# Kernel tuning notes

Hardware: AMD Instinct MI355X
Metric: run time of the kernel (lower is better)

## Reference

```python
import jax, jax.numpy as jnp
import numpy as np
import math

D = 1024
H = 16

def setup_inputs() -> dict:
    key = jax.random.key(0)
    ks = jax.random.split(key, 8)
    N, X, T = 2, 1024, 4096
    s = 1.0 / math.sqrt(D)
    return {
        "previous_output": jax.random.normal(ks[0], (N, X, D), jnp.float32),
        "context": jax.random.normal(ks[1], (N, T, D), jnp.float32),
        "Wq": jax.random.normal(ks[2], (D, D), jnp.float32) * s,
        "bq": jnp.zeros((D,), jnp.float32),
        "Wk": jax.random.normal(ks[3], (D, D), jnp.float32) * s,
        "bk": jnp.zeros((D,), jnp.float32),
        "Wv": jax.random.normal(ks[4], (D, D), jnp.float32) * s,
        "bv": jnp.zeros((D,), jnp.float32),
    }

def reference(previous_output, context, Wq, bq, Wk, bk, Wv, bv):
    N, X, _ = previous_output.shape
    T = context.shape[1]
    hd = D // H
    # linear projections (torch Linear: x @ W.T + b)
    q = (previous_output @ Wq.T + bq).reshape(N, X, H, hd).transpose(0, 2, 1, 3)  # (N,H,X,hd)
    k = (context @ Wk.T + bk).reshape(N, T, H, hd).transpose(0, 2, 1, 3)          # (N,H,T,hd)
    v = (context @ Wv.T + bv).reshape(N, T, H, hd).transpose(0, 2, 1, 3)          # (N,H,T,hd)
    scores = jnp.einsum('nhxd,nhtd->nhxt', q, k) / jnp.sqrt(jnp.float32(hd))       # (N,H,X,T)
    attn = jax.nn.softmax(scores, axis=-1)
    out = jnp.einsum('nhxt,nhtd->nhxd', attn, v)                                   # (N,H,X,hd)
    return out.transpose(0, 2, 1, 3).reshape(N, X, D)
```

## Files before the change

### kernel.cpp

```cpp
#include <hip/hip_runtime.h>

typedef __bf16 bf16_t;
typedef __bf16 bf16x8 __attribute__((ext_vector_type(8)));
typedef __bf16 bf16x4 __attribute__((ext_vector_type(4)));
typedef float f32x4 __attribute__((ext_vector_type(4)));

#define D_MODEL 1024
#define NHEAD 16
#define HD 64
#define XLEN 1024
#define TLEN 4096
#define NBATCH 2
#define CEXP 0.18033688011112042f

typedef __attribute__((address_space(3))) bf16_t lds_bf16;
typedef const __attribute__((address_space(1))) bf16_t glb_bf16;

__global__ __launch_bounds__(256) void convert5(const float* __restrict__ prev, const float* __restrict__ ctx,
                                                const float* __restrict__ wq, const float* __restrict__ wk,
                                                const float* __restrict__ wv,
                                                bf16_t* __restrict__ prev_b, bf16_t* __restrict__ ctx_b,
                                                bf16_t* __restrict__ wq_b, bf16_t* __restrict__ wk_b,
                                                bf16_t* __restrict__ wv_b) {
    int b = blockIdx.x;
    const float* src; bf16_t* dst; int lb;
    if (b < 256)       { src = prev; dst = prev_b; lb = b; }
    else if (b < 1280) { src = ctx;  dst = ctx_b;  lb = b - 256; }
    else if (b < 1408) { src = wq;   dst = wq_b;   lb = b - 1280; }
    else if (b < 1536) { src = wk;   dst = wk_b;   lb = b - 1408; }
    else               { src = wv;   dst = wv_b;   lb = b - 1536; }
    const int base = lb * 8192 + threadIdx.x * 4;
#pragma unroll
    for (int i = 0; i < 8; ++i) {
        const int off = base + i * 1024;
        f32x4 f = *(const f32x4*)(src + off);
        bf16x4 h;
        h[0] = (bf16_t)f[0]; h[1] = (bf16_t)f[1]; h[2] = (bf16_t)f[2]; h[3] = (bf16_t)f[3];
        *(bf16x4*)(dst + off) = h;
    }
}

__global__ __launch_bounds__(256) void gemm_fused(const bf16_t* __restrict__ Xq, const bf16_t* __restrict__ Xc,
                                                  const bf16_t* __restrict__ wq, const bf16_t* __restrict__ wk,
                                                  const bf16_t* __restrict__ wv,
                                                  const float* __restrict__ bq, const float* __restrict__ bk,
                                                  const float* __restrict__ bv,
                                                  bf16_t* __restrict__ Qh, bf16_t* __restrict__ Kh,
                                                  bf16_t* __restrict__ Vt) {
    __shared__ bf16_t Ab[128][32];
    __shared__ bf16_t Bb[128][32];

    const int tid  = threadIdx.x;
    const int w    = tid >> 6;
    const int lane = tid & 63;
    const int q4   = lane >> 4;
    const int c    = lane & 15;

    const bf16_t* X; const bf16_t* W; const float* bias;
    int m0, n0, lshift, vmode;
    const int bid = blockIdx.x;
    if (bid < 128) {
        X = Xq; W = wq; bias = bq; lshift = 10; vmode = 0;
        m0 = (bid >> 3) * 128; n0 = (bid & 7) * 128;
    } else {
        const int b = bid - 128;
        const int xcd  = b & 7;
        const int s    = b >> 3;
        const int nb   = s >> 3;
        const int mgrp = s & 7;
        m0 = (mgrp * 8 + xcd) * 128;
        X = Xc; lshift = 12;
        if (nb < 8) { W = wk; bias = bk; vmode = 0; n0 = nb * 128; }
        else        { W = wv; bias = bv; vmode = 1; n0 = (nb - 8) * 128; }
    }
    const float osc = (bid < 128) ? CEXP : 1.0f;

    f32x4 acc[4][4];
#pragma unroll
    for (int i = 0; i < 4; ++i)
#pragma unroll
        for (int j = 0; j < 4; ++j) acc[i][j] = (f32x4){0.f, 0.f, 0.f, 0.f};

    const int mq = (w & 1) * 64;
    const int nq = (w >> 1) * 64;

    bf16_t* aBase = &Ab[0][0] + w * 512;
    bf16_t* bBase = &Bb[0][0] + w * 512;
    const bf16_t* gA = X + (size_t)(m0 + (tid >> 2)) * D_MODEL + (tid & 3) * 8;
    const bf16_t* gB = W + (size_t)(n0 + (tid >> 2)) * D_MODEL + (tid & 3) * 8;

    for (int kk = 0; kk < D_MODEL; kk += 32) {
        __syncthreads();
        __builtin_amdgcn_global_load_lds((glb_bf16*)(gA + kk), (lds_bf16*)aBase, 16, 0, 0);
        __builtin_amdgcn_global_load_lds((glb_bf16*)(gA + kk + (size_t)64 * D_MODEL), (lds_bf16*)(aBase + 2048), 16, 0, 0);
        __builtin_amdgcn_global_load_lds((glb_bf16*)(gB + kk), (lds_bf16*)bBase, 16, 0, 0);
        __builtin_amdgcn_global_load_lds((glb_bf16*)(gB + kk + (size_t)64 * D_MODEL), (lds_bf16*)(bBase + 2048), 16, 0, 0);
        __syncthreads();

        bf16x8 a[4], b[4];
#pragma unroll
        for (int i = 0; i < 4; ++i) a[i] = *(const bf16x8*)&Ab[mq + i * 16 + c][q4 * 8];
#pragma unroll
        for (int i = 0; i < 4; ++i) b[i] = *(const bf16x8*)&Bb[nq + i * 16 + c][q4 * 8];
#pragma unroll
        for (int mi = 0; mi < 4; ++mi)
#pragma unroll
            for (int ni = 0; ni < 4; ++ni)
                acc[mi][ni] = __builtin_amdgcn_mfma_f32_16x16x32_bf16(a[mi], b[ni], acc[mi][ni], 0, 0, 0);
    }

    float bv4[4];
#pragma unroll
    for (int ni = 0; ni < 4; ++ni) bv4[ni] = bias[n0 + nq + ni * 16 + c];

    const int headbase = (n0 + nq) >> 6;
    if (vmode == 0) {
        bf16_t* OutQK = (bid < 128) ? Qh : Kh;
        const int L = 1 << lshift;
#pragma unroll
        for (int mi = 0; mi < 4; ++mi) {
            const int mrow = m0 + mq + mi * 16 + q4 * 4;
            const int nb2  = mrow >> lshift;
            const int pos  = mrow & (L - 1);
            bf16_t* ob = OutQK + ((size_t)(nb2 * NHEAD + headbase) * L + pos) * HD;
#pragma unroll
            for (int ni = 0; ni < 4; ++ni) {
                const int d = ni * 16 + c;
#pragma unroll
                for (int r = 0; r < 4; ++r)
                    ob[(size_t)r * HD + d] = (bf16_t)((acc[mi][ni][r] + bv4[ni]) * osc);
            }
        }
    } else {
#pragma unroll
        for (int mi = 0; mi < 4; ++mi) {
            const int mrow = m0 + mq + mi * 16 + q4 * 4;
            const int nb2  = mrow >> 12;
            const int pos  = mrow & 4095;
            const int lin  = (pos & ~31) + ((pos >> 2) & 3) * 8 + ((pos >> 4) & 1) * 4;
#pragma unroll
            for (int ni = 0; ni < 4; ++ni) {
                const int d = ni * 16 + c;
                bf16x4 v4;
#pragma unroll
                for (int r = 0; r < 4; ++r) v4[r] = (bf16_t)(acc[mi][ni][r] + bv4[ni]);
                *(bf16x4*)(Vt + ((size_t)(nb2 * NHEAD + headbase) * HD + d) * TLEN + lin) = v4;
            }
        }
    }
}

__global__ __launch_bounds__(256, 4) void attn_kernel(const bf16_t* __restrict__ Qh,
                                                      const bf16_t* __restrict__ Kh,
                                                      const bf16_t* __restrict__ Vt,
                                                      bf16_t* __restrict__ Opart,
                                                      float* __restrict__ Lpart) {
    __shared__ __align__(16) char smem[32768];

    const int tid  = threadIdx.x;
    const int lane = tid & 63;
    const int w    = tid >> 6;
    const int q4   = lane >> 4;
    const int c    = lane & 15;

    const int bid = blockIdx.x;
    const int xcd = bid & 7;
    const int seq = bid >> 3;
    const int tq  = seq & 3;
    const int xb  = (seq >> 2) & 7;
    const int g   = seq >> 5;
    const int nh  = g * 8 + xcd;
    const int xw  = xb * 128 + w * 32;

    const bf16_t* __restrict__ Kb = Kh + (size_t)nh * TLEN * HD;
    const bf16_t* __restrict__ Vb = Vt + (size_t)nh * HD * TLEN;

    bf16x8 qa[2][2];
#pragma unroll
    for (int mi = 0; mi < 2; ++mi) {
        const bf16_t* qr = Qh + ((size_t)nh * XLEN + xw + mi * 16 + c) * HD + q4 * 8;
        qa[mi][0] = *(const bf16x8*)(qr);
        qa[mi][1] = *(const bf16x8*)(qr + 32);
    }

    const int sRow0 = tid >> 3,  sRow1 = 32 + (tid >> 3);
    const int sCh   = tid & 7;
    const int kCol0 = ((sCh ^ (sRow0 & 7)) * 8);
    const int kCol1 = ((sCh ^ (sRow1 & 7)) * 8);

    const int ofs0 = c * 128 + ((q4 ^ (c & 7)) * 16);
    const int ofs1 = c * 128 + (((4 + q4) ^ (c & 7)) * 16);

    f32x4 o[2][4];
#pragma unroll
    for (int i = 0; i < 2; ++i)
#pragma unroll
        for (int j = 0; j < 4; ++j) o[i][j] = (f32x4){0.f, 0.f, 0.f, 0.f};
    f32x4 lacc[2];
    lacc[0] = (f32x4){0.f, 0.f, 0.f, 0.f};
    lacc[1] = (f32x4){0.f, 0.f, 0.f, 0.f};

    bf16x8 ones8;
#pragma unroll
    for (int j = 0; j < 8; ++j) ones8[j] = (bf16_t)1.0f;

    const int t0base = tq * (TLEN / 4);

    {
        bf16_t* base = (bf16_t*)smem;
        __builtin_amdgcn_global_load_lds((glb_bf16*)(Kb + (size_t)(t0base + sRow0) * HD + kCol0), (lds_bf16*)(base + w * 512), 16, 0, 0);
        __builtin_amdgcn_global_load_lds((glb_bf16*)(Kb + (size_t)(t0base + sRow1) * HD + kCol1), (lds_bf16*)(base + 2048 + w * 512), 16, 0, 0);
        __builtin_amdgcn_global_load_lds((glb_bf16*)(Vb + (size_t)sRow0 * TLEN + t0base + kCol0), (lds_bf16*)(base + 4096 + w * 512), 16, 0, 0);
        __builtin_amdgcn_global_load_lds((glb_bf16*)(Vb + (size_t)sRow1 * TLEN + t0base + kCol1), (lds_bf16*)(base + 6144 + w * 512), 16, 0, 0);
    }

    for (int s = 0; s < 16; ++s) {
        __syncthreads();
        if (s < 15) {
            const int t1 = t0base + (s + 1) * 64;
            bf16_t* base = (bf16_t*)smem + ((s + 1) & 1) * 8192;
            __builtin_amdgcn_global_load_lds((glb_bf16*)(Kb + (size_t)(t1 + sRow0) * HD + kCol0), (lds_bf16*)(base + w * 512), 16, 0, 0);
            __builtin_amdgcn_global_load_lds((glb_bf16*)(Kb + (size_t)(t1 + sRow1) * HD + kCol1), (lds_bf16*)(base + 2048 + w * 512), 16, 0, 0);
            __builtin_amdgcn_global_load_lds((glb_bf16*)(Vb + (size_t)sRow0 * TLEN + t1 + kCol0), (lds_bf16*)(base + 4096 + w * 512), 16, 0, 0);
            __builtin_amdgcn_global_load_lds((glb_bf16*)(Vb + (size_t)sRow1 * TLEN + t1 + kCol1), (lds_bf16*)(base + 6144 + w * 512), 16, 0, 0);
        }

        const char* KtB = smem + (s & 1) * 16384;
        const char* VsB = KtB + 8192;
#pragma unroll
        for (int g32 = 0; g32 < 2; ++g32) {
            bf16x8 p8[2];
#pragma unroll
            for (int tt = 0; tt < 2; ++tt) {
                const int rofs = g32 * 4096 + tt * 2048;
                bf16x8 kb0 = *(const bf16x8*)(KtB + rofs + ofs0);
                bf16x8 kb1 = *(const bf16x8*)(KtB + rofs + ofs1);
#pragma unroll
                for (int mi = 0; mi < 2; ++mi) {
                    f32x4 sv = (f32x4){0.f, 0.f, 0.f, 0.f};
                    sv = __builtin_amdgcn_mfma_f32_16x16x32_bf16(kb0, qa[mi][0], sv, 0, 0, 0);
                    sv = __builtin_amdgcn_mfma_f32_16x16x32_bf16(kb1, qa[mi][1], sv, 0, 0, 0);
#pragma unroll
                    for (int r = 0; r < 4; ++r)
                        p8[mi][tt * 4 + r] = (bf16_t)__builtin_exp2f(sv[r]);
                }
            }
            const int vsel = g32 ? ofs1 : ofs0;
            bf16x8 va[4];
#pragma unroll
            for (int dt = 0; dt < 4; ++dt)
                va[dt] = *(const bf16x8*)(VsB + vsel + dt * 2048);
#pragma unroll
            for (int mi = 0; mi < 2; ++mi) {
#pragma unroll
                for (int dt = 0; dt < 4; ++dt)
                    o[mi][dt] = __builtin_amdgcn_mfma_f32_16x16x32_bf16(va[dt], p8[mi], o[mi][dt], 0, 0, 0);
                lacc[mi] = __builtin_amdgcn_mfma_f32_16x16x32_bf16(ones8, p8[mi], lacc[mi], 0, 0, 0);
            }
        }
    }

    __syncthreads();
    bf16_t* Ob = (bf16_t*)smem;
    float*  Lb = (float*)(smem + 16896);
#pragma unroll
    for (int mi = 0; mi < 2; ++mi) {
        if (q4 == 0) Lb[w * 32 + mi * 16 + c] = lacc[mi][0];
#pragma unroll
        for (int dt = 0; dt < 4; ++dt)
#pragma unroll
            for (int r = 0; r < 4; ++r)
                Ob[w * 2112 + (dt * 16 + q4 * 4 + r) * 33 + mi * 16 + c] = (bf16_t)o[mi][dt][r];
    }
    {
        const int lr = lane >> 1;
        const int dh = lane & 1;
        bf16x8 out4[4];
#pragma unroll
        for (int j2 = 0; j2 < 4; ++j2)
#pragma unroll
            for (int e = 0; e < 8; ++e)
                out4[j2][e] = Ob[w * 2112 + (dh * 32 + j2 * 8 + e) * 33 + lr];
        const size_t pair = (size_t)nh * XLEN + xw + lr;
        bf16_t* op = Opart + (pair * 4 + tq) * HD + dh * 32;
#pragma unroll
        for (int j2 = 0; j2 < 4; ++j2)
            *(bf16x8*)(op + j2 * 8) = out4[j2];
        if (dh == 0) Lpart[pair * 4 + tq] = Lb[w * 32 + lr];
    }
}

__global__ __launch_bounds__(256) void attn_merge(const bf16_t* __restrict__ Opart,
                                                  const float* __restrict__ Lpart,
                                                  float* __restrict__ Out) {
    const int u    = blockIdx.x * 256 + threadIdx.x;
    const int pair = u >> 3;
    const int d0   = (u & 7) * 8;
    const int nh   = pair >> 10;
    const int x    = pair & 1023;
    const int n    = nh >> 4;
    const int h    = nh & 15;

    float l = 0.f;
    float s[8];
#pragma unroll
    for (int j = 0; j < 8; ++j) s[j] = 0.f;
#pragma unroll
    for (int tqi = 0; tqi < 4; ++tqi) {
        l += Lpart[pair * 4 + tqi];
        bf16x8 v = *(const bf16x8*)(Opart + ((size_t)pair * 4 + tqi) * HD + d0);
#pragma unroll
        for (int j = 0; j < 8; ++j) s[j] += (float)v[j];
    }
    const float inv = 1.0f / l;
    f32x4 v0, v1;
#pragma unroll
    for (int j = 0; j < 4; ++j) { v0[j] = s[j] * inv; v1[j] = s[4 + j] * inv; }
    float* op = Out + ((size_t)(n * XLEN + x)) * D_MODEL + h * HD + d0;
    *(f32x4*)(op)     = v0;
    *(f32x4*)(op + 4) = v1;
}

extern "C" void kernel_launch(void* const* d_in, const int* in_sizes, int n_in,
                              void* d_out, int out_size, void* d_ws, size_t ws_size,
                              hipStream_t stream) {
    (void)in_sizes; (void)n_in; (void)out_size; (void)ws_size;
    const float* prev = (const float*)d_in[0];
    const float* ctx  = (const float*)d_in[1];
    const float* Wq   = (const float*)d_in[2];
    const float* bq   = (const float*)d_in[3];
    const float* Wk   = (const float*)d_in[4];
    const float* bk   = (const float*)d_in[5];
    const float* Wv   = (const float*)d_in[6];
    const float* bv   = (const float*)d_in[7];

    const size_t MiB = 1024 * 1024;
    char* ws = (char*)d_ws;
    bf16_t* prev_b = (bf16_t*)(ws);
    bf16_t* ctx_b  = (bf16_t*)(ws + 4 * MiB);
    bf16_t* wq_b   = (bf16_t*)(ws + 20 * MiB);
    bf16_t* wk_b   = (bf16_t*)(ws + 22 * MiB);
    bf16_t* wv_b   = (bf16_t*)(ws + 24 * MiB);
    bf16_t* Qh     = (bf16_t*)(ws + 26 * MiB);
    bf16_t* Kh     = (bf16_t*)(ws + 30 * MiB);
    bf16_t* Vt     = (bf16_t*)(ws + 46 * MiB);
    bf16_t* Opart  = ctx_b;
    float*  Lpart  = (float*)prev_b;

    convert5<<<1664, 256, 0, stream>>>(prev, ctx, Wq, Wk, Wv, prev_b, ctx_b, wq_b, wk_b, wv_b);
    gemm_fused<<<128 + 1024, 256, 0, stream>>>(prev_b, ctx_b, wq_b, wk_b, wv_b, bq, bk, bv, Qh, Kh, Vt);
    attn_kernel<<<1024, 256, 0, stream>>>(Qh, Kh, Vt, Opart, Lpart);
    attn_merge<<<1024, 256, 0, stream>>>(Opart, Lpart, (float*)d_out);
}
```

Measured before the change: 209.6 us.

## Double-buffer projection GEMM LDS tiles with XOR-swizzled layout

The fused QKV projection GEMM gets a two-stage LDS ping-pong buffer. The global-to-LDS loads for the next K tile are issued before the MFMAs on the current tile, and one barrier per iteration replaces two. The LDS layout also gets an XOR swizzle on the 16-byte chunk index, applied on both the load and the read side, to cut bank conflicts. The cost is twice the LDS per block, which may lower occupancy, and the code now depends on the LDS-DMA completion being waited on correctly before the reads.

```diff
diff --git a/kernel.cpp b/kernel.cpp
--- a/kernel.cpp
+++ b/kernel.cpp
@@ -47,8 +47,7 @@
                                                   const float* __restrict__ bv,
                                                   bf16_t* __restrict__ Qh, bf16_t* __restrict__ Kh,
                                                   bf16_t* __restrict__ Vt) {
-    __shared__ bf16_t Ab[128][32];
-    __shared__ bf16_t Bb[128][32];
+    __shared__ __align__(16) char smem[32768];
 
     const int tid  = threadIdx.x;
     const int w    = tid >> 6;
@@ -84,24 +83,45 @@
     const int mq = (w & 1) * 64;
     const int nq = (w >> 1) * 64;
 
-    bf16_t* aBase = &Ab[0][0] + w * 512;
-    bf16_t* bBase = &Bb[0][0] + w * 512;
-    const bf16_t* gA = X + (size_t)(m0 + (tid >> 2)) * D_MODEL + (tid & 3) * 8;
-    const bf16_t* gB = W + (size_t)(n0 + (tid >> 2)) * D_MODEL + (tid & 3) * 8;
-
-    for (int kk = 0; kk < D_MODEL; kk += 32) {
+    const int jl = (tid & 3) ^ ((tid >> 3) & 3);
+    const bf16_t* gA = X + (size_t)(m0 + (tid >> 2)) * D_MODEL + jl * 8;
+    const bf16_t* gB = W + (size_t)(n0 + (tid >> 2)) * D_MODEL + jl * 8;
+    const int ldsSlot = w * 512;
+
+    const int pj = (c >> 1) & 3;
+    int aofs[4], bofs[4];
+#pragma unroll
+    for (int i = 0; i < 4; ++i) {
+        aofs[i] = (mq + i * 16 + c) * 64 + ((q4 ^ pj) * 16);
+        bofs[i] = (nq + i * 16 + c) * 64 + ((q4 ^ pj) * 16);
+    }
+
+    {
+        bf16_t* base = (bf16_t*)smem;
+        __builtin_amdgcn_global_load_lds((glb_bf16*)(gA), (lds_bf16*)(base + ldsSlot), 16, 0, 0);
+        __builtin_amdgcn_global_load_lds((glb_bf16*)(gA + (size_t)64 * D_MODEL), (lds_bf16*)(base + 2048 + ldsSlot), 16, 0, 0);
+        __builtin_amdgcn_global_load_lds((glb_bf16*)(gB), (lds_bf16*)(base + 4096 + ldsSlot), 16, 0, 0);
+        __builtin_amdgcn_global_load_lds((glb_bf16*)(gB + (size_t)64 * D_MODEL), (lds_bf16*)(base + 6144 + ldsSlot), 16, 0, 0);
+    }
+
+    for (int ki = 0; ki < 32; ++ki) {
         __syncthreads();
-        __builtin_amdgcn_global_load_lds((glb_bf16*)(gA + kk), (lds_bf16*)aBase, 16, 0, 0);
-        __builtin_amdgcn_global_load_lds((glb_bf16*)(gA + kk + (size_t)64 * D_MODEL), (lds_bf16*)(aBase + 2048), 16, 0, 0);
-        __builtin_amdgcn_global_load_lds((glb_bf16*)(gB + kk), (lds_bf16*)bBase, 16, 0, 0);
-        __builtin_amdgcn_global_load_lds((glb_bf16*)(gB + kk + (size_t)64 * D_MODEL), (lds_bf16*)(bBase + 2048), 16, 0, 0);
-        __syncthreads();
+        if (ki < 31) {
+            const int kk = (ki + 1) * 32;
+            bf16_t* base = (bf16_t*)smem + ((ki + 1) & 1) * 8192;
+            __builtin_amdgcn_global_load_lds((glb_bf16*)(gA + kk), (lds_bf16*)(base + ldsSlot), 16, 0, 0);
+            __builtin_amdgcn_global_load_lds((glb_bf16*)(gA + kk + (size_t)64 * D_MODEL), (lds_bf16*)(base + 2048 + ldsSlot), 16, 0, 0);
+            __builtin_amdgcn_global_load_lds((glb_bf16*)(gB + kk), (lds_bf16*)(base + 4096 + ldsSlot), 16, 0, 0);
+            __builtin_amdgcn_global_load_lds((glb_bf16*)(gB + kk + (size_t)64 * D_MODEL), (lds_bf16*)(base + 6144 + ldsSlot), 16, 0, 0);
+        }
+        const char* Abuf = smem + (ki & 1) * 16384;
+        const char* Bbuf = Abuf + 8192;
 
         bf16x8 a[4], b[4];
 #pragma unroll
-        for (int i = 0; i < 4; ++i) a[i] = *(const bf16x8*)&Ab[mq + i * 16 + c][q4 * 8];
-#pragma unroll
-        for (int i = 0; i < 4; ++i) b[i] = *(const bf16x8*)&Bb[nq + i * 16 + c][q4 * 8];
+        for (int i = 0; i < 4; ++i) a[i] = *(const bf16x8*)(Abuf + aofs[i]);
+#pragma unroll
+        for (int i = 0; i < 4; ++i) b[i] = *(const bf16x8*)(Bbuf + bofs[i]);
 #pragma unroll
         for (int mi = 0; mi < 4; ++mi)
 #pragma unroll
```

Result: no change. 213.6 us (+1.9%).
